# Performance work log

Measured on AMD Instinct MI355X. Metric: run time of the kernel, lower is better.

## Reference

```python
import jax, jax.numpy as jnp
import numpy as np

D_MODEL = 1024
N_HEADS = 16
HEAD_DIM = D_MODEL // N_HEADS
B, S = 4, 2048


def setup_inputs() -> dict:
    key = jax.random.key(0)
    ks = jax.random.split(key, 12)
    s = 1.0 / np.sqrt(D_MODEL)
    inp = {
        'query': jax.random.normal(ks[0], (B, S, D_MODEL), jnp.float32),
        'key': jax.random.normal(ks[1], (B, S, D_MODEL), jnp.float32),
        'value': jax.random.normal(ks[2], (B, S, D_MODEL), jnp.float32),
        # causal mask, broadcast over batch and heads: [1,1,S,S]
        'mask': jnp.tril(jnp.ones((S, S), jnp.int32))[None, None],
        'Wq': jax.random.normal(ks[3], (D_MODEL, D_MODEL), jnp.float32) * s,
        'bq': jnp.zeros((D_MODEL,), jnp.float32),
        'Wk': jax.random.normal(ks[4], (D_MODEL, D_MODEL), jnp.float32) * s,
        'bk': jnp.zeros((D_MODEL,), jnp.float32),
        'Wv': jax.random.normal(ks[5], (D_MODEL, D_MODEL), jnp.float32) * s,
        'bv': jnp.zeros((D_MODEL,), jnp.float32),
        'Wo': jax.random.normal(ks[6], (D_MODEL, D_MODEL), jnp.float32) * s,
        'bo': jnp.zeros((D_MODEL,), jnp.float32),
    }
    return inp


def reference(query, key, value, mask, Wq, bq, Wk, bk, Wv, bv, Wo, bo):
    b, q_len, _ = query.shape
    scale = jnp.sqrt(jnp.float32(HEAD_DIM))
    # projections
    q = query @ Wq + bq
    k = key @ Wk + bk
    v = value @ Wv + bv
    # [b, h, s, hd]
    q = q.reshape(b, q_len, N_HEADS, HEAD_DIM).transpose(0, 2, 1, 3)
    k = k.reshape(b, -1, N_HEADS, HEAD_DIM).transpose(0, 2, 1, 3)
    v = v.reshape(b, -1, N_HEADS, HEAD_DIM).transpose(0, 2, 1, 3)
    scores = jnp.einsum('bhqd,bhkd->bhqk', q, k) / scale
    scores = jnp.where(mask == 0, jnp.float32(-jnp.inf), scores)
    attn = jax.nn.softmax(scores, axis=-1)  # dropout p=0 / eval mode
    out = jnp.einsum('bhqk,bhkd->bhqd', attn, v)
    out = out.transpose(0, 2, 1, 3).reshape(b, q_len, D_MODEL)
    return out @ Wo + bo
```

## Files before the change

kernel.cpp:

```cpp
#include <hip/hip_runtime.h>
#include <hip/hip_bf16.h>

typedef __attribute__((ext_vector_type(8))) short short8;
typedef __attribute__((ext_vector_type(4))) float floatx4;
typedef __attribute__((ext_vector_type(4))) unsigned short ushort4v;

#define D_MODEL 1024
#define S_LEN   2048
#define N_HEADS 16
#define HEAD_DIM 64
#define BATCH   4

__device__ __forceinline__ unsigned short f2bf(float x) {
    union { float f; unsigned int u; } v; v.f = x;
    unsigned int u = v.u;
    unsigned int r = (u + 0x7FFFu + ((u >> 16) & 1u)) >> 16;
    return (unsigned short)r;
}
__device__ __forceinline__ unsigned short f2bf_trunc(float x) {
    union { float f; unsigned int u; } v; v.f = x;
    return (unsigned short)(v.u >> 16);
}

__device__ __forceinline__ void gload_lds16(const void* g, void* s) {
    __builtin_amdgcn_global_load_lds(
        (const __attribute__((address_space(1))) void*)g,
        (__attribute__((address_space(3))) void*)s, 16, 0, 0);
}

struct Conv3 {
    const float* src[3];
    unsigned short* dst[3];
};

__global__ __launch_bounds__(256) void conv_bf16(Conv3 a) {
    const float* s = a.src[blockIdx.z];
    unsigned short* d = a.dst[blockIdx.z];
    size_t i = ((size_t)blockIdx.x * 256 + threadIdx.x) * 8;
    float4 f0 = *(const float4*)(s + i);
    float4 f1 = *(const float4*)(s + i + 4);
    short8 v;
    v[0] = (short)f2bf(f0.x); v[1] = (short)f2bf(f0.y);
    v[2] = (short)f2bf(f0.z); v[3] = (short)f2bf(f0.w);
    v[4] = (short)f2bf(f1.x); v[5] = (short)f2bf(f1.y);
    v[6] = (short)f2bf(f1.z); v[7] = (short)f2bf(f1.w);
    *(short8*)(d + i) = v;
}

struct Trans4 {
    const float* W[4];
    unsigned short* Wt[4];
};

__global__ __launch_bounds__(256) void transpose_w(Trans4 args) {
    __shared__ unsigned short tile[32][33];
    const float* W = args.W[blockIdx.z];
    unsigned short* Wt = args.Wt[blockIdx.z];
    int n0 = blockIdx.x * 32;
    int k0 = blockIdx.y * 32;
    int t = threadIdx.x;
    int r = t >> 5, c = t & 31;
    for (int i = 0; i < 4; ++i) {
        int k = k0 + r + i * 8;
        tile[r + i * 8][c] = f2bf(W[(size_t)k * D_MODEL + n0 + c]);
    }
    __syncthreads();
    for (int i = 0; i < 4; ++i) {
        int n = n0 + r + i * 8;
        Wt[(size_t)n * D_MODEL + k0 + c] = tile[c][r + i * 8];
    }
}

struct GemmIn {
    const unsigned short* A;
    const unsigned short* Bt;
    const float* bias;
    void* C;
    int mode;
    float scale;
};
struct Gemm3 { GemmIn g[3]; };

#define BAR()   asm volatile("s_barrier" ::: "memory")
#define VMW4()  asm volatile("s_waitcnt vmcnt(4)" ::: "memory")
#define VMW2()  asm volatile("s_waitcnt vmcnt(2)" ::: "memory")
#define VMW0()  asm volatile("s_waitcnt vmcnt(0)" ::: "memory")

#define READ_AB_S(BUF, KS)                                                     \
    _Pragma("unroll") for (int ii = 0; ii < 4; ++ii)                           \
        aF[ii][KS] = *(const short8*)&lds[(BUF)*16384 + aOff + ii*512 + (KS)*4096]; \
    _Pragma("unroll") for (int jj = 0; jj < 4; ++jj)                           \
        bF[jj][KS] = *(const short8*)&lds[(BUF)*16384 + bOff + jj*512 + (KS)*4096];
#define MFMA_S(KS)                                                             \
    _Pragma("unroll") for (int ii = 0; ii < 4; ++ii)                           \
    _Pragma("unroll") for (int jj = 0; jj < 4; ++jj)                           \
        acc[ii][jj] = __builtin_amdgcn_mfma_f32_16x16x32_bf16(                 \
            aF[ii][KS], bF[jj][KS], acc[ii][jj], 0, 0, 0);

__global__ __launch_bounds__(256, 2) void gemm_128(Gemm3 args) {
    constexpr int K = D_MODEL, N = D_MODEL;
    constexpr int NT = K / 64;
    GemmIn g = args.g[blockIdx.z];

    __shared__ __align__(16) unsigned short lds[32768];

    const int m0 = blockIdx.x * 128;
    const int n0 = blockIdx.y * 128;
    const int t = threadIdx.x;
    const int w = t >> 6, lane = t & 63;
    const int quad = lane >> 4, l16 = lane & 15;
    const int wm = w >> 1, wn = w & 1;

    const int srow = w * 32 + (lane >> 2);
    const int scol = ((lane & 3) * 8) ^ ((lane & 32) ? 16 : 0);

    const int fx = (quad * 8) ^ ((l16 & 8) ? 16 : 0);
    const int aOff = (wm * 64 + l16) * 32 + fx;
    const int bOff = 8192 + (wn * 64 + l16) * 32 + fx;

    floatx4 acc[4][4] = {};
    short8 aF[4][2], bF[4][2];

    auto stageA = [&](int buf, int kt) {
        const unsigned short* s0 = g.A + (size_t)(m0 + srow) * K + kt * 64 + scol;
        unsigned short* d0 = &lds[buf * 16384 + (w * 32) * 32];
        gload_lds16(s0, d0);
        gload_lds16(s0 + 32, d0 + 4096);
        gload_lds16(s0 + (size_t)16 * K, d0 + 512);
        gload_lds16(s0 + (size_t)16 * K + 32, d0 + 512 + 4096);
    };
    auto stageB = [&](int buf, int kt) {
        const unsigned short* s0 = g.Bt + (size_t)(n0 + srow) * K + kt * 64 + scol;
        unsigned short* d0 = &lds[buf * 16384 + 8192 + (w * 32) * 32];
        gload_lds16(s0, d0);
        gload_lds16(s0 + 32, d0 + 4096);
        gload_lds16(s0 + (size_t)16 * K, d0 + 512);
        gload_lds16(s0 + (size_t)16 * K + 32, d0 + 512 + 4096);
    };

    stageA(0, 0); stageB(0, 0);
    VMW0();
    BAR();

#pragma unroll 2
    for (int kt = 0; kt < NT; ++kt) {
        const int buf = kt & 1;
        if (kt + 1 < NT) { stageA(buf ^ 1, kt + 1); stageB(buf ^ 1, kt + 1); }
        READ_AB_S(buf, 0);
        READ_AB_S(buf, 1);
        MFMA_S(0);
        MFMA_S(1);
        if (kt + 1 < NT) { VMW0(); BAR(); }
    }

    if (g.mode == 2) {
        unsigned short* Ct = (unsigned short*)g.C;
#pragma unroll
        for (int j = 0; j < 4; ++j) {
            int col = n0 + wn * 64 + j * 16 + l16;
            int h = col >> 6, dd = col & 63;
            float bv = g.bias[col];
#pragma unroll
            for (int i = 0; i < 4; ++i) {
                int row0 = m0 + wm * 64 + i * 16 + quad * 4;
                int bb = row0 >> 11, s = row0 & 2047;
                ushort4v u;
#pragma unroll
                for (int r = 0; r < 4; ++r) u[r] = f2bf((acc[i][j][r] + bv) * g.scale);
                *(ushort4v*)(Ct + ((size_t)(bb * 16 + h) * 64 + dd) * 2048 + s) = u;
            }
        }
    } else {
#pragma unroll
        for (int j = 0; j < 4; ++j) {
            int col = n0 + wn * 64 + j * 16 + l16;
            float bv = g.bias[col];
#pragma unroll
            for (int i = 0; i < 4; ++i) {
#pragma unroll
                for (int r = 0; r < 4; ++r) {
                    int row = m0 + wm * 64 + i * 16 + quad * 4 + r;
                    float v = (acc[i][j][r] + bv) * g.scale;
                    if (g.mode == 1)
                        ((float*)g.C)[(size_t)row * N + col] = v;
                    else
                        ((unsigned short*)g.C)[(size_t)row * N + col] = f2bf(v);
                }
            }
        }
    }
}

__global__ __launch_bounds__(512) void flash_attn(
    const unsigned short* __restrict__ Qp,
    const unsigned short* __restrict__ Kp,
    const unsigned short* __restrict__ Vtg,
    unsigned short* __restrict__ Op) {
    constexpr int S = S_LEN, D = D_MODEL;
    __shared__ __align__(16) unsigned short Ks[3 * 4096];
    __shared__ __align__(16) unsigned short Vs[3 * 4096];
    __shared__ __align__(16) unsigned short Ps[8][1024];

    int id = blockIdx.x + (blockIdx.y << 3);
    int pair = (id >> 3) & 7;
    int bh = (id & 7) | ((id >> 6) << 3);
    int b = bh >> 4;
    int t = threadIdx.x;
    int wave = t >> 6, lane = t & 63;
    int quad = lane >> 4, l16 = lane & 15;

    const size_t head_off = (size_t)b * S * D + (size_t)(bh & 15) * HEAD_DIM;
    const unsigned short* Khead = Kp + head_off;
    const unsigned short* Vhead = Vtg + (size_t)bh * 64 * S;

    int q0l = pair * 128, q0h = (15 - pair) * 128;
    int qgl = q0l + wave * 16 + l16;
    int qgh = q0h + wave * 16 + l16;

    const unsigned short* qpl = Qp + head_off + (size_t)qgl * D + quad * 8;
    short8 ql0 = *(const short8*)qpl, ql1 = *(const short8*)(qpl + 32);
    const unsigned short* qph = Qp + head_off + (size_t)qgh * D + quad * 8;
    short8 qh0 = *(const short8*)qph, qh1 = *(const short8*)(qph + 32);

    floatx4 ol[4] = {}, oh[4] = {};
    floatx4 lsl = {}, lsh = {};

    short8 a1;
#pragma unroll
    for (int e = 0; e < 8; ++e) a1[e] = (l16 == 0) ? (short)0x3F80 : (short)0;

    int sw = wave & 3;
    bool doK = wave < 4;
    int srow = sw * 16 + (lane >> 2);
    int scol = ((lane & 3) * 8) ^ ((lane & 32) ? 16 : 0);

    auto stage = [&](int buf, int k0) {
        if (doK) {
            const unsigned short* s0 = Khead + (size_t)(k0 + srow) * D + scol;
            unsigned short* d0 = Ks + buf * 4096 + sw * 512;
            gload_lds16(s0, d0);
            gload_lds16(s0 + 32, d0 + 2048);
        } else {
            const unsigned short* s0 = Vhead + (size_t)srow * S + k0 + scol;
            unsigned short* d0 = Vs + buf * 4096 + sw * 512;
            gload_lds16(s0, d0);
            gload_lds16(s0 + 32, d0 + 2048);
        }
    };

    int wqminl = q0l + wave * 16, wqmaxl = wqminl + 15;
    int wqminh = q0h + wave * 16, wqmaxh = wqminh + 15;

    const int swz = (quad * 8) ^ ((l16 & 8) ? 16 : 0);
    const int pswz = (l16 & 8) ? 16 : 0;
    unsigned short* pw = &Ps[wave][0];

    auto half_step = [&](const unsigned short* Kb, const unsigned short* Vb,
                         int k0, int qg, int wqmin, floatx4& ls,
                         floatx4* o, short8 qb0, short8 qb1) {
        floatx4 st[4];
        __builtin_amdgcn_s_setprio(1);
        for (int gk = 0; gk < 4; ++gk) {
            short8 ka0 = *(const short8*)&Kb[(gk * 16 + l16) * 32 + swz];
            short8 ka1 = *(const short8*)&Kb[2048 + (gk * 16 + l16) * 32 + swz];
            floatx4 s = {};
            s = __builtin_amdgcn_mfma_f32_16x16x32_bf16(ka0, qb0, s, 0, 0, 0);
            s = __builtin_amdgcn_mfma_f32_16x16x32_bf16(ka1, qb1, s, 0, 0, 0);
            st[gk] = s;
        }
        __builtin_amdgcn_s_setprio(0);

        float sv[16];
        if (k0 + 63 < wqmin) {
            for (int i = 0; i < 16; ++i)
                sv[i] = __builtin_amdgcn_exp2f(st[i >> 2][i & 3]);
        } else {
            for (int gk = 0; gk < 4; ++gk)
                for (int r = 0; r < 4; ++r) {
                    int key = k0 + gk * 16 + quad * 4 + r;
                    sv[gk * 4 + r] = (key <= qg)
                        ? __builtin_amdgcn_exp2f(st[gk][r]) : 0.f;
                }
        }

        for (int gk = 0; gk < 4; ++gk) {
            ushort4v u;
            for (int r = 0; r < 4; ++r) u[r] = f2bf_trunc(sv[gk * 4 + r]);
            *(ushort4v*)&pw[(gk >> 1) * 512 + l16 * 32 +
                            ((((gk & 1) * 16) + quad * 4) ^ pswz)] = u;
        }

        short8 pf0 = *(const short8*)&pw[l16 * 32 + swz];
        short8 pf1 = *(const short8*)&pw[512 + l16 * 32 + swz];
        __builtin_amdgcn_s_setprio(1);
        ls = __builtin_amdgcn_mfma_f32_16x16x32_bf16(a1, pf0, ls, 0, 0, 0);
        ls = __builtin_amdgcn_mfma_f32_16x16x32_bf16(a1, pf1, ls, 0, 0, 0);
        for (int jd = 0; jd < 4; ++jd) {
            short8 va0 = *(const short8*)&Vb[(jd * 16 + l16) * 32 + swz];
            short8 va1 = *(const short8*)&Vb[2048 + (jd * 16 + l16) * 32 + swz];
            o[jd] = __builtin_amdgcn_mfma_f32_16x16x32_bf16(va0, pf0, o[jd], 0, 0, 0);
            o[jd] = __builtin_amdgcn_mfma_f32_16x16x32_bf16(va1, pf1, o[jd], 0, 0, 0);
        }
        __builtin_amdgcn_s_setprio(0);
    };

    int n_kt = 2 * (15 - pair) + 2;
    stage(0, 0);
    stage(1, 64);
    for (int kt = 0; kt < n_kt; ++kt) {
        int k0 = kt * 64;
        if (kt + 2 < n_kt) {
            stage((kt + 2) % 3, k0 + 128);
            VMW4();
        } else if (kt + 1 < n_kt) {
            VMW2();
        } else {
            VMW0();
        }
        BAR();

        const unsigned short* Kb = Ks + (kt % 3) * 4096;
        const unsigned short* Vb = Vs + (kt % 3) * 4096;
        if (k0 <= wqmaxl) half_step(Kb, Vb, k0, qgl, wqminl, lsl, ol, ql0, ql1);
        if (k0 <= wqmaxh) half_step(Kb, Vb, k0, qgh, wqminh, lsh, oh, qh0, qh1);
        BAR();
    }

    {
        float inv = 1.0f / __shfl(lsl[0], l16);
        unsigned short* op = Op + head_off + (size_t)qgl * D;
        for (int jd = 0; jd < 4; ++jd) {
            ushort4v u;
            for (int r = 0; r < 4; ++r) u[r] = f2bf(ol[jd][r] * inv);
            *(ushort4v*)(op + jd * 16 + quad * 4) = u;
        }
    }
    {
        float inv = 1.0f / __shfl(lsh[0], l16);
        unsigned short* op = Op + head_off + (size_t)qgh * D;
        for (int jd = 0; jd < 4; ++jd) {
            ushort4v u;
            for (int r = 0; r < 4; ++r) u[r] = f2bf(oh[jd][r] * inv);
            *(ushort4v*)(op + jd * 16 + quad * 4) = u;
        }
    }
}

extern "C" void kernel_launch(void* const* d_in, const int* in_sizes, int n_in,
                              void* d_out, int out_size, void* d_ws,
                              size_t ws_size, hipStream_t stream) {
    const float* query = (const float*)d_in[0];
    const float* key   = (const float*)d_in[1];
    const float* value = (const float*)d_in[2];
    const float* Wq = (const float*)d_in[4];
    const float* bq = (const float*)d_in[5];
    const float* Wk = (const float*)d_in[6];
    const float* bk = (const float*)d_in[7];
    const float* Wv = (const float*)d_in[8];
    const float* bv = (const float*)d_in[9];
    const float* Wo = (const float*)d_in[10];
    const float* bo = (const float*)d_in[11];
    float* out = (float*)d_out;

    char* ws = (char*)d_ws;
    const size_t WT_SZ = (size_t)D_MODEL * D_MODEL * 2;
    const size_t X_SZ = (size_t)BATCH * S_LEN * D_MODEL * 2;
    unsigned short* wtq = (unsigned short*)(ws);
    unsigned short* wtk = (unsigned short*)(ws + WT_SZ);
    unsigned short* wtv = (unsigned short*)(ws + 2 * WT_SZ);
    unsigned short* wto = (unsigned short*)(ws + 3 * WT_SZ);
    unsigned short* Qbf = (unsigned short*)(ws + 4 * WT_SZ);
    unsigned short* Kbf = (unsigned short*)(ws + 4 * WT_SZ + X_SZ);
    unsigned short* Vbf = (unsigned short*)(ws + 4 * WT_SZ + 2 * X_SZ);
    unsigned short* Qp  = (unsigned short*)(ws + 4 * WT_SZ + 3 * X_SZ);
    unsigned short* Kp  = (unsigned short*)(ws + 4 * WT_SZ + 4 * X_SZ);
    unsigned short* Vtg = (unsigned short*)(ws + 4 * WT_SZ + 5 * X_SZ);
    unsigned short* Ao  = Qbf;

    Trans4 ta;
    ta.W[0] = Wq; ta.W[1] = Wk; ta.W[2] = Wv; ta.W[3] = Wo;
    ta.Wt[0] = wtq; ta.Wt[1] = wtk; ta.Wt[2] = wtv; ta.Wt[3] = wto;
    transpose_w<<<dim3(32, 32, 4), 256, 0, stream>>>(ta);

    Conv3 ca;
    ca.src[0] = query; ca.src[1] = key; ca.src[2] = value;
    ca.dst[0] = Qbf;   ca.dst[1] = Kbf; ca.dst[2] = Vbf;
    conv_bf16<<<dim3(4096, 1, 3), 256, 0, stream>>>(ca);

    const float q_scale = 0.125f * 1.44269504088896340736f;
    Gemm3 gq;
    gq.g[0].A = Qbf; gq.g[0].Bt = wtq; gq.g[0].bias = bq; gq.g[0].C = Qp;  gq.g[0].mode = 0; gq.g[0].scale = q_scale;
    gq.g[1].A = Kbf; gq.g[1].Bt = wtk; gq.g[1].bias = bk; gq.g[1].C = Kp;  gq.g[1].mode = 0; gq.g[1].scale = 1.0f;
    gq.g[2].A = Vbf; gq.g[2].Bt = wtv; gq.g[2].bias = bv; gq.g[2].C = Vtg; gq.g[2].mode = 2; gq.g[2].scale = 1.0f;
    gemm_128<<<dim3(64, 8, 3), 256, 0, stream>>>(gq);

    flash_attn<<<dim3(8, BATCH * N_HEADS), 512, 0, stream>>>(
        Qp, Kp, Vtg, Ao);

    Gemm3 go;
    go.g[0].A = Ao; go.g[0].Bt = wto; go.g[0].bias = bo; go.g[0].C = out; go.g[0].mode = 1; go.g[0].scale = 1.0f;
    gemm_128<<<dim3(64, 8, 1), 256, 0, stream>>>(go);
}
```

Measured before the change: 322.1 us.

## Share K/V LDS fragment loads across both query halves and batch GEMM fragment reads

The attention loop now reads the K and V fragments from LDS once per key tile and reuses them for both the low and high query halves, instead of reloading them inside each half_step call. The two halves' QK and softmax stages run first, followed by both PV stages. In the projection GEMM, all A/B fragment reads are issued together, then an explicit lgkmcnt(0) wait, then all MFMAs under raised wave priority. The aim is to cut LDS traffic and raise MFMA issue density, at the cost of more live registers (kv array, both P fragments) and less interleaving of LDS reads with MFMAs in the GEMM.

```diff
diff --git a/kernel.cpp b/kernel.cpp
--- a/kernel.cpp
+++ b/kernel.cpp
@@ -82,20 +82,31 @@
 struct Gemm3 { GemmIn g[3]; };
 
 #define BAR()   asm volatile("s_barrier" ::: "memory")
+#define LGKM0() asm volatile("s_waitcnt lgkmcnt(0)" ::: "memory")
 #define VMW4()  asm volatile("s_waitcnt vmcnt(4)" ::: "memory")
 #define VMW2()  asm volatile("s_waitcnt vmcnt(2)" ::: "memory")
 #define VMW0()  asm volatile("s_waitcnt vmcnt(0)" ::: "memory")
 
-#define READ_AB_S(BUF, KS)                                                     \
+#define READ_A4(BUF)                                                           \
+    _Pragma("unroll") for (int ii = 0; ii < 4; ++ii) {                         \
+        aF[ii][0] = *(const short8*)&lds[(BUF)*16384 + aOff + ii*512];         \
+        aF[ii][1] = *(const short8*)&lds[(BUF)*16384 + aOff + ii*512 + 4096];  \
+    }
+#define READ_B4(BUF)                                                           \
+    _Pragma("unroll") for (int jj = 0; jj < 4; ++jj) {                         \
+        bF[jj][0] = *(const short8*)&lds[(BUF)*16384 + bOff + jj*512];         \
+        bF[jj][1] = *(const short8*)&lds[(BUF)*16384 + bOff + jj*512 + 4096];  \
+    }
+#define MFMA_ALL()                                                             \
+    __builtin_amdgcn_s_setprio(1);                                             \
     _Pragma("unroll") for (int ii = 0; ii < 4; ++ii)                           \
-        aF[ii][KS] = *(const short8*)&lds[(BUF)*16384 + aOff + ii*512 + (KS)*4096]; \
-    _Pragma("unroll") for (int jj = 0; jj < 4; ++jj)                           \
-        bF[jj][KS] = *(const short8*)&lds[(BUF)*16384 + bOff + jj*512 + (KS)*4096];
-#define MFMA_S(KS)                                                             \
-    _Pragma("unroll") for (int ii = 0; ii < 4; ++ii)                           \
-    _Pragma("unroll") for (int jj = 0; jj < 4; ++jj)                           \
+    _Pragma("unroll") for (int jj = 0; jj < 4; ++jj) {                         \
         acc[ii][jj] = __builtin_amdgcn_mfma_f32_16x16x32_bf16(                 \
-            aF[ii][KS], bF[jj][KS], acc[ii][jj], 0, 0, 0);
+            aF[ii][0], bF[jj][0], acc[ii][jj], 0, 0, 0);                       \
+        acc[ii][jj] = __builtin_amdgcn_mfma_f32_16x16x32_bf16(                 \
+            aF[ii][1], bF[jj][1], acc[ii][jj], 0, 0, 0);                       \
+    }                                                                          \
+    __builtin_amdgcn_s_setprio(0)
 
 __global__ __launch_bounds__(256, 2) void gemm_128(Gemm3 args) {
     constexpr int K = D_MODEL, N = D_MODEL;
@@ -146,10 +157,9 @@
     for (int kt = 0; kt < NT; ++kt) {
         const int buf = kt & 1;
         if (kt + 1 < NT) { stageA(buf ^ 1, kt + 1); stageB(buf ^ 1, kt + 1); }
-        READ_AB_S(buf, 0);
-        READ_AB_S(buf, 1);
-        MFMA_S(0);
-        MFMA_S(1);
+        READ_A4(buf); READ_B4(buf);
+        LGKM0();
+        MFMA_ALL();
         if (kt + 1 < NT) { VMW0(); BAR(); }
     }
 
@@ -255,53 +265,33 @@
     const int pswz = (l16 & 8) ? 16 : 0;
     unsigned short* pw = &Ps[wave][0];
 
-    auto half_step = [&](const unsigned short* Kb, const unsigned short* Vb,
-                         int k0, int qg, int wqmin, floatx4& ls,
-                         floatx4* o, short8 qb0, short8 qb1) {
-        floatx4 st[4];
-        __builtin_amdgcn_s_setprio(1);
-        for (int gk = 0; gk < 4; ++gk) {
-            short8 ka0 = *(const short8*)&Kb[(gk * 16 + l16) * 32 + swz];
-            short8 ka1 = *(const short8*)&Kb[2048 + (gk * 16 + l16) * 32 + swz];
-            floatx4 s = {};
-            s = __builtin_amdgcn_mfma_f32_16x16x32_bf16(ka0, qb0, s, 0, 0, 0);
-            s = __builtin_amdgcn_mfma_f32_16x16x32_bf16(ka1, qb1, s, 0, 0, 0);
-            st[gk] = s;
-        }
-        __builtin_amdgcn_s_setprio(0);
-
+    auto softmax_pf = [&](floatx4* st, int k0, int qg, int wqmin,
+                          short8& pf0, short8& pf1) {
         float sv[16];
         if (k0 + 63 < wqmin) {
+#pragma unroll
             for (int i = 0; i < 16; ++i)
                 sv[i] = __builtin_amdgcn_exp2f(st[i >> 2][i & 3]);
         } else {
+#pragma unroll
             for (int gk = 0; gk < 4; ++gk)
+#pragma unroll
                 for (int r = 0; r < 4; ++r) {
                     int key = k0 + gk * 16 + quad * 4 + r;
                     sv[gk * 4 + r] = (key <= qg)
                         ? __builtin_amdgcn_exp2f(st[gk][r]) : 0.f;
                 }
         }
-
+#pragma unroll
         for (int gk = 0; gk < 4; ++gk) {
             ushort4v u;
+#pragma unroll
             for (int r = 0; r < 4; ++r) u[r] = f2bf_trunc(sv[gk * 4 + r]);
             *(ushort4v*)&pw[(gk >> 1) * 512 + l16 * 32 +
                             ((((gk & 1) * 16) + quad * 4) ^ pswz)] = u;
         }
-
-        short8 pf0 = *(const short8*)&pw[l16 * 32 + swz];
-        short8 pf1 = *(const short8*)&pw[512 + l16 * 32 + swz];
-        __builtin_amdgcn_s_setprio(1);
-        ls = __builtin_amdgcn_mfma_f32_16x16x32_bf16(a1, pf0, ls, 0, 0, 0);
-        ls = __builtin_amdgcn_mfma_f32_16x16x32_bf16(a1, pf1, ls, 0, 0, 0);
-        for (int jd = 0; jd < 4; ++jd) {
-            short8 va0 = *(const short8*)&Vb[(jd * 16 + l16) * 32 + swz];
-            short8 va1 = *(const short8*)&Vb[2048 + (jd * 16 + l16) * 32 + swz];
-            o[jd] = __builtin_amdgcn_mfma_f32_16x16x32_bf16(va0, pf0, o[jd], 0, 0, 0);
-            o[jd] = __builtin_amdgcn_mfma_f32_16x16x32_bf16(va1, pf1, o[jd], 0, 0, 0);
-        }
-        __builtin_amdgcn_s_setprio(0);
+        pf0 = *(const short8*)&pw[l16 * 32 + swz];
+        pf1 = *(const short8*)&pw[512 + l16 * 32 + swz];
     };
 
     int n_kt = 2 * (15 - pair) + 2;
@@ -321,8 +311,69 @@
 
         const unsigned short* Kb = Ks + (kt % 3) * 4096;
         const unsigned short* Vb = Vs + (kt % 3) * 4096;
-        if (k0 <= wqmaxl) half_step(Kb, Vb, k0, qgl, wqminl, lsl, ol, ql0, ql1);
-        if (k0 <= wqmaxh) half_step(Kb, Vb, k0, qgh, wqminh, lsh, oh, qh0, qh1);
+        const bool doL = k0 <= wqmaxl;
+        const bool doH = k0 <= wqmaxh;
+
+        short8 kv[8];
+#pragma unroll
+        for (int gk = 0; gk < 4; ++gk) {
+            kv[gk * 2]     = *(const short8*)&Kb[(gk * 16 + l16) * 32 + swz];
+            kv[gk * 2 + 1] = *(const short8*)&Kb[2048 + (gk * 16 + l16) * 32 + swz];
+        }
+        short8 pfl0, pfl1, pfh0, pfh1;
+        if (doL) {
+            floatx4 st[4];
+            __builtin_amdgcn_s_setprio(1);
+#pragma unroll
+            for (int gk = 0; gk < 4; ++gk) {
+                floatx4 s = {};
+                s = __builtin_amdgcn_mfma_f32_16x16x32_bf16(kv[gk * 2], ql0, s, 0, 0, 0);
+                s = __builtin_amdgcn_mfma_f32_16x16x32_bf16(kv[gk * 2 + 1], ql1, s, 0, 0, 0);
+                st[gk] = s;
+            }
+            __builtin_amdgcn_s_setprio(0);
+            softmax_pf(st, k0, qgl, wqminl, pfl0, pfl1);
+        }
+        if (doH) {
+            floatx4 st[4];
+            __builtin_amdgcn_s_setprio(1);
+#pragma unroll
+            for (int gk = 0; gk < 4; ++gk) {
+                floatx4 s = {};
+                s = __builtin_amdgcn_mfma_f32_16x16x32_bf16(kv[gk * 2], qh0, s, 0, 0, 0);
+                s = __builtin_amdgcn_mfma_f32_16x16x32_bf16(kv[gk * 2 + 1], qh1, s, 0, 0, 0);
+                st[gk] = s;
+            }
+            __builtin_amdgcn_s_setprio(0);
+            softmax_pf(st, k0, qgh, wqminh, pfh0, pfh1);
+        }
+
+#pragma unroll
+        for (int jd = 0; jd < 4; ++jd) {
+            kv[jd * 2]     = *(const short8*)&Vb[(jd * 16 + l16) * 32 + swz];
+            kv[jd * 2 + 1] = *(const short8*)&Vb[2048 + (jd * 16 + l16) * 32 + swz];
+        }
+        __builtin_amdgcn_s_setprio(1);
+        if (doL) {
+            lsl = __builtin_amdgcn_mfma_f32_16x16x32_bf16(a1, pfl0, lsl, 0, 0, 0);
+            lsl = __builtin_amdgcn_mfma_f32_16x16x32_bf16(a1, pfl1, lsl, 0, 0, 0);
+#pragma unroll
+            for (int jd = 0; jd < 4; ++jd) {
+                ol[jd] = __builtin_amdgcn_mfma_f32_16x16x32_bf16(kv[jd * 2], pfl0, ol[jd], 0, 0, 0);
+                ol[jd] = __builtin_amdgcn_mfma_f32_16x16x32_bf16(kv[jd * 2 + 1], pfl1, ol[jd], 0, 0, 0);
+            }
+        }
+        if (doH) {
+            lsh = __builtin_amdgcn_mfma_f32_16x16x32_bf16(a1, pfh0, lsh, 0, 0, 0);
+            lsh = __builtin_amdgcn_mfma_f32_16x16x32_bf16(a1, pfh1, lsh, 0, 0, 0);
+#pragma unroll
+            for (int jd = 0; jd < 4; ++jd) {
+                oh[jd] = __builtin_amdgcn_mfma_f32_16x16x32_bf16(kv[jd * 2], pfh0, oh[jd], 0, 0, 0);
+                oh[jd] = __builtin_amdgcn_mfma_f32_16x16x32_bf16(kv[jd * 2 + 1], pfh1, oh[jd], 0, 0, 0);
+            }
+        }
+        __builtin_amdgcn_s_setprio(0);
+
         BAR();
     }
 
```

After: 328.5 us. Within noise of the previous version (+2.0%).

## Restructure GEMM LDS reads with priority MFMA block; shrink attention K/V ring to double buffer

Applied to the files above, without the earlier changes.

In the GEMM, all A/B fragments for both k-substeps are now loaded from LDS up front, followed by an explicit lgkmcnt(0) wait. All MFMAs then issue together inside an s_setprio(1) region, with the two k-substeps interleaved per accumulator. In flash attention, the K/V staging ring drops from three LDS buffers to two, prefetching one tile ahead instead of two, which cuts LDS use and may raise occupancy. The cost is less prefetch depth, so global-load latency may be exposed in attention, and the explicit wait removes compiler freedom to overlap LDS reads with MFMAs.

```diff
diff --git a/kernel.cpp b/kernel.cpp
--- a/kernel.cpp
+++ b/kernel.cpp
@@ -82,20 +82,30 @@
 struct Gemm3 { GemmIn g[3]; };
 
 #define BAR()   asm volatile("s_barrier" ::: "memory")
-#define VMW4()  asm volatile("s_waitcnt vmcnt(4)" ::: "memory")
+#define LGKM0() asm volatile("s_waitcnt lgkmcnt(0)" ::: "memory")
 #define VMW2()  asm volatile("s_waitcnt vmcnt(2)" ::: "memory")
 #define VMW0()  asm volatile("s_waitcnt vmcnt(0)" ::: "memory")
 
-#define READ_AB_S(BUF, KS)                                                     \
+#define READ_A4(BUF)                                                           \
+    _Pragma("unroll") for (int ii = 0; ii < 4; ++ii) {                         \
+        aF[ii][0] = *(const short8*)&lds[(BUF)*16384 + aOff + ii*512];         \
+        aF[ii][1] = *(const short8*)&lds[(BUF)*16384 + aOff + ii*512 + 4096];  \
+    }
+#define READ_B4(BUF)                                                           \
+    _Pragma("unroll") for (int jj = 0; jj < 4; ++jj) {                         \
+        bF[jj][0] = *(const short8*)&lds[(BUF)*16384 + bOff + jj*512];         \
+        bF[jj][1] = *(const short8*)&lds[(BUF)*16384 + bOff + jj*512 + 4096];  \
+    }
+#define MFMA_ALL()                                                             \
+    __builtin_amdgcn_s_setprio(1);                                             \
     _Pragma("unroll") for (int ii = 0; ii < 4; ++ii)                           \
-        aF[ii][KS] = *(const short8*)&lds[(BUF)*16384 + aOff + ii*512 + (KS)*4096]; \
-    _Pragma("unroll") for (int jj = 0; jj < 4; ++jj)                           \
-        bF[jj][KS] = *(const short8*)&lds[(BUF)*16384 + bOff + jj*512 + (KS)*4096];
-#define MFMA_S(KS)                                                             \
-    _Pragma("unroll") for (int ii = 0; ii < 4; ++ii)                           \
-    _Pragma("unroll") for (int jj = 0; jj < 4; ++jj)                           \
+    _Pragma("unroll") for (int jj = 0; jj < 4; ++jj) {                         \
         acc[ii][jj] = __builtin_amdgcn_mfma_f32_16x16x32_bf16(                 \
-            aF[ii][KS], bF[jj][KS], acc[ii][jj], 0, 0, 0);
+            aF[ii][0], bF[jj][0], acc[ii][jj], 0, 0, 0);                       \
+        acc[ii][jj] = __builtin_amdgcn_mfma_f32_16x16x32_bf16(                 \
+            aF[ii][1], bF[jj][1], acc[ii][jj], 0, 0, 0);                       \
+    }                                                                          \
+    __builtin_amdgcn_s_setprio(0)
 
 __global__ __launch_bounds__(256, 2) void gemm_128(Gemm3 args) {
     constexpr int K = D_MODEL, N = D_MODEL;
@@ -146,10 +156,9 @@
     for (int kt = 0; kt < NT; ++kt) {
         const int buf = kt & 1;
         if (kt + 1 < NT) { stageA(buf ^ 1, kt + 1); stageB(buf ^ 1, kt + 1); }
-        READ_AB_S(buf, 0);
-        READ_AB_S(buf, 1);
-        MFMA_S(0);
-        MFMA_S(1);
+        READ_A4(buf); READ_B4(buf);
+        LGKM0();
+        MFMA_ALL();
         if (kt + 1 < NT) { VMW0(); BAR(); }
     }
 
@@ -197,8 +206,8 @@
     const unsigned short* __restrict__ Vtg,
     unsigned short* __restrict__ Op) {
     constexpr int S = S_LEN, D = D_MODEL;
-    __shared__ __align__(16) unsigned short Ks[3 * 4096];
-    __shared__ __align__(16) unsigned short Vs[3 * 4096];
+    __shared__ __align__(16) unsigned short Ks[2 * 4096];
+    __shared__ __align__(16) unsigned short Vs[2 * 4096];
     __shared__ __align__(16) unsigned short Ps[8][1024];
 
     int id = blockIdx.x + (blockIdx.y << 3);
@@ -306,21 +315,18 @@
 
     int n_kt = 2 * (15 - pair) + 2;
     stage(0, 0);
-    stage(1, 64);
     for (int kt = 0; kt < n_kt; ++kt) {
         int k0 = kt * 64;
-        if (kt + 2 < n_kt) {
-            stage((kt + 2) % 3, k0 + 128);
-            VMW4();
-        } else if (kt + 1 < n_kt) {
+        if (kt + 1 < n_kt) {
+            stage((kt + 1) & 1, k0 + 64);
             VMW2();
         } else {
             VMW0();
         }
         BAR();
 
-        const unsigned short* Kb = Ks + (kt % 3) * 4096;
-        const unsigned short* Vb = Vs + (kt % 3) * 4096;
+        const unsigned short* Kb = Ks + (kt & 1) * 4096;
+        const unsigned short* Vb = Vs + (kt & 1) * 4096;
         if (k0 <= wqmaxl) half_step(Kb, Vb, k0, qgl, wqminl, lsl, ol, ql0, ql1);
         if (k0 <= wqmaxh) half_step(Kb, Vb, k0, qgh, wqminh, lsh, oh, qh0, qh1);
         BAR();
```

New measurement: 312.8 us. 2.9% less time.
